# Kernel tuning notes

Measured on AMD Instinct MI355X. Metric: run time of the kernel, lower is better.

The kernel has to match this reference:

```python
import jax, jax.numpy as jnp
import numpy as np

B, C, D = 512, 100000, 512
MARGIN = 0.5  # ArcFace-style additive angular margin


def setup_inputs() -> dict:
    key = jax.random.key(0)
    k1, k2, k3 = jax.random.split(key, 3)
    embeddings = jax.random.normal(k1, (B, D), dtype=jnp.float32)
    labels = jax.random.randint(k2, (B,), 0, C, dtype=jnp.int32)
    weight = 0.01 * jax.random.normal(k3, (C, D), dtype=jnp.float32)  # torch.normal(0, 0.01, (C, D))
    return {"embeddings": embeddings, "labels": labels, "weight": weight}


def _l2_normalize(x, eps=1e-12):
    return x / jnp.maximum(jnp.linalg.norm(x, axis=-1, keepdims=True), eps)


def reference(embeddings, labels, weight):
    cos_m = jnp.cos(MARGIN)
    sin_m = jnp.sin(MARGIN)

    e = _l2_normalize(embeddings)          # (B, D)
    w = _l2_normalize(weight)              # (C, D)
    logits = jnp.clip(jnp.einsum('bd,cd->bc', e, w), -1.0, 1.0)  # (B, C) cosines

    bsz, ncls = logits.shape
    rows = jnp.arange(bsz)
    cos_t = logits[rows, labels]                                   # (B,) cos(theta_y)
    sin_t = jnp.sqrt(jnp.clip(1.0 - cos_t * cos_t, 0.0, None))     # sin(theta_y)
    cos_tm = cos_t * cos_m - sin_t * sin_m                         # cos(theta_y + m)
    sin_tm = sin_t * cos_m + cos_t * sin_m                         # sin(theta_y + m)

    # non-target class indices per row, ascending, skipping the target: (B, C-1)
    base = jnp.arange(ncls - 1)[None, :]
    nt_idx = base + (base >= labels[:, None]).astype(base.dtype)

    # margin_softmax: logits2 = cos(theta_j) - cos(theta_y + m) over non-target j
    nt_logits = jnp.take_along_axis(logits, nt_idx, axis=1)       # (B, C-1)
    logits2 = nt_logits - cos_tm[:, None]

    # no_grad block: weight_m is unit-norm point at angle theta_y+m from e,
    # so ||w_j - w_m||^2 = 2 - 2 <w_j, w_m>  (avoids materializing (B, C, D)).
    w_y = w[labels]                                                # (B, D)
    w_m = (-sin_m * e + sin_tm[:, None] * w_y) / sin_t[:, None]    # (B, D), unit norm
    sim = jnp.einsum('bd,cd->bc', w_m, w)                          # (B, C)
    nt_sim = jnp.take_along_axis(sim, nt_idx, axis=1)              # (B, C-1)
    diff_weight_norm = jax.lax.stop_gradient(
        jnp.sqrt(jnp.clip(2.0 - 2.0 * nt_sim, 0.0, None)))         # (B, C-1)

    e_logits = jnp.sum(jnp.exp(logits2 / diff_weight_norm), axis=1)  # (B,)
    return jnp.mean(jnp.log1p(e_logits))
```

## Files before the change

kernel.cpp:

```cpp
#include <hip/hip_runtime.h>
#include <hip/hip_fp8.h>
#include <math.h>

#define B_SZ 512
#define C_SZ 100000
#define D_SZ 512

#define BM 128
#define BN 128
#define BK 64
#define NTILES 782
#define MT 8
#define NBLK (NTILES * MT)
#define KSTEPS 8
#define DEPTH 3

typedef __attribute__((ext_vector_type(4))) float f32x4;
typedef __attribute__((ext_vector_type(16))) float f32x16;
typedef __attribute__((ext_vector_type(4))) int i32x4;
typedef __attribute__((ext_vector_type(8))) int i32x8;

#define UNITY_SCALE 0x7F7F7F7F

__device__ __forceinline__ void gload_lds16(const void* gptr, void* lptr) {
  __builtin_amdgcn_global_load_lds(
      (const __attribute__((address_space(1))) void*)gptr,
      (__attribute__((address_space(3))) void*)lptr,
      16, 0, 0);
}

__device__ __forceinline__ unsigned char f2fp8(float x) {
  __hip_fp8_e4m3 h(x);
  return (unsigned char)h.__x;
}
__device__ __forceinline__ float fp82f(unsigned int u) {
  __hip_fp8_e4m3 h;
  h.__x = (unsigned char)u;
  return (float)h;
}
__device__ __forceinline__ unsigned int pack4f8(float a, float b, float c, float d) {
  return (unsigned int)f2fp8(a) | ((unsigned int)f2fp8(b) << 8) |
         ((unsigned int)f2fp8(c) << 16) | ((unsigned int)f2fp8(d) << 24);
}

__global__ __launch_bounds__(256) void k_norm_w(const float* __restrict__ w,
                                                unsigned char* __restrict__ w8) {
  const int row = blockIdx.x * 4 + (threadIdx.x >> 6);
  const int lane = threadIdx.x & 63;
  const float4* wr = (const float4*)(w + (size_t)row * D_SZ);
  float4 v0 = wr[lane];
  float4 v1 = wr[64 + lane];
  float ss = v0.x*v0.x + v0.y*v0.y + v0.z*v0.z + v0.w*v0.w
           + v1.x*v1.x + v1.y*v1.y + v1.z*v1.z + v1.w*v1.w;
  #pragma unroll
  for (int o = 32; o; o >>= 1) ss += __shfl_xor(ss, o, 64);
  const float rn = __builtin_amdgcn_rsqf(fmaxf(ss, 1e-24f));
  unsigned int* out = (unsigned int*)(w8 + (size_t)row * D_SZ);
  out[lane] = pack4f8(v0.x * rn, v0.y * rn, v0.z * rn, v0.w * rn);
  out[64 + lane] = pack4f8(v1.x * rn, v1.y * rn, v1.z * rn, v1.w * rn);
}

__global__ __launch_bounds__(64) void k_prep(const float* __restrict__ e,
                                             const int* __restrict__ labels,
                                             const unsigned char* __restrict__ w8,
                                             unsigned char* __restrict__ A8,
                                             float4* __restrict__ params) {
  const int b = blockIdx.x;
  const int lane = threadIdx.x;
  const float4* er = (const float4*)(e + (size_t)b * D_SZ);
  float4 v0 = er[lane], v1 = er[64 + lane];
  float ss = v0.x*v0.x + v0.y*v0.y + v0.z*v0.z + v0.w*v0.w
           + v1.x*v1.x + v1.y*v1.y + v1.z*v1.z + v1.w*v1.w;
  #pragma unroll
  for (int o = 32; o; o >>= 1) ss += __shfl_xor(ss, o, 64);
  const float rn = __builtin_amdgcn_rsqf(fmaxf(ss, 1e-24f));
  v0.x *= rn; v0.y *= rn; v0.z *= rn; v0.w *= rn;
  v1.x *= rn; v1.y *= rn; v1.z *= rn; v1.w *= rn;

  unsigned int* arow_e = (unsigned int*)(A8 + (size_t)(2 * b) * D_SZ);
  arow_e[lane] = pack4f8(v0.x, v0.y, v0.z, v0.w);
  arow_e[64 + lane] = pack4f8(v1.x, v1.y, v1.z, v1.w);

  const int lab = labels[b];
  const unsigned int* wr = (const unsigned int*)(w8 + (size_t)lab * D_SZ);
  unsigned int w0 = wr[lane], w1 = wr[64 + lane];
  unsigned int* arow_w = (unsigned int*)(A8 + (size_t)(2 * b + 1) * D_SZ);
  arow_w[lane] = w0;
  arow_w[64 + lane] = w1;

  float d = v0.x * fp82f(w0 & 255) + v0.y * fp82f((w0 >> 8) & 255)
          + v0.z * fp82f((w0 >> 16) & 255) + v0.w * fp82f(w0 >> 24)
          + v1.x * fp82f(w1 & 255) + v1.y * fp82f((w1 >> 8) & 255)
          + v1.z * fp82f((w1 >> 16) & 255) + v1.w * fp82f(w1 >> 24);
  #pragma unroll
  for (int o = 32; o; o >>= 1) d += __shfl_xor(d, o, 64);

  if (lane == 0) {
    const float cos_m = 0.877582561890372716f;
    const float sin_m = 0.479425538604203000f;
    float cos_t = fminf(fmaxf(d, -1.0f), 1.0f);
    float sin_t = sqrtf(fmaxf(1.0f - cos_t * cos_t, 0.0f));
    float cos_tm = cos_t * cos_m - sin_t * sin_m;
    float sin_tm = sin_t * cos_m + cos_t * sin_m;
    float inv_st = 1.0f / fmaxf(sin_t, 1e-20f);
    params[b] = make_float4(cos_tm, sin_m * inv_st, sin_tm * inv_st, 0.0f);
  }
}

__device__ __forceinline__ float termf(float de, float dwy, float4 p, bool kill) {
  float c = fminf(fmaxf(de, -1.0f), 1.0f);
  float s = p.z * dwy - p.y * de;
  float x = fmaxf(fmaf(-2.0f, s, 2.0f), 1e-20f);
  float t = (c - p.x) * __builtin_amdgcn_rsqf(x);
  float r = __expf(t);
  return kill ? 0.0f : r;
}

__global__ __launch_bounds__(512, 4) void k_gemm(const unsigned char* __restrict__ A8,
                                                 const unsigned char* __restrict__ W8,
                                                 const float4* __restrict__ params,
                                                 const int* __restrict__ labels,
                                                 float* __restrict__ part) {
  __shared__ __align__(32) unsigned char At[DEPTH][BM * BK];
  __shared__ __align__(32) unsigned char Bt[DEPTH][BN * BK];
  __shared__ float ered[64];
  __shared__ float4 pl[64];
  __shared__ int ll[64];

  const int bid = blockIdx.x;
  const int p = (bid & 7) * (NBLK / 8) + (bid >> 3);
  const int nt = p >> 3, mt = p & 7;
  const int t = threadIdx.x;
  const int w = t >> 6, l = t & 63;
  const int m0 = mt * BM;
  const int n0 = nt * BN;
  const int b0 = mt * 64;

  if (t < 64) {
    ered[t] = 0.0f;
    pl[t] = params[b0 + t];
    ll[t] = labels[b0 + t];
  }

  const int kpart = ((t >> 5) & 1) * 32 + ((t >> 6) & 1) * 16;
  const int aoffs = (m0 + (t >> 7) * 32 + (t & 31)) * D_SZ + kpart;
  int brow_s = n0 + (t >> 7) * 32 + (t & 31);
  if (brow_s >= C_SZ) brow_s = C_SZ - 1;
  const int boffs = brow_s * D_SZ + kpart;

  f32x16 accA = {}, accB = {};
  const int fA = w & 3;
  const int fB0 = (w >> 2) * 2;
  const int hi = l >> 5;

#define STAGE(d, ts)                                                        \
  do {                                                                      \
    const int k0_ = (ts) * BK;                                              \
    gload_lds16(A8 + aoffs + k0_, (void*)(At[d] + t * 16));                 \
    gload_lds16(W8 + (size_t)(boffs + k0_), (void*)(Bt[d] + t * 16));       \
  } while (0)

  STAGE(0, 0);
  STAGE(1, 1);
  STAGE(2, 2);
  asm volatile("s_waitcnt vmcnt(4) lgkmcnt(0)" ::: "memory");
  __builtin_amdgcn_s_barrier();

  #pragma unroll
  for (int step = 0; step < KSTEPS; ++step) {
    const int d = step % DEPTH;
    i32x4 alo = *(const i32x4*)(At[d] + fA * 2048 + l * 16);
    i32x4 ahi = *(const i32x4*)(At[d] + fA * 2048 + 1024 + l * 16);
    i32x8 av = __builtin_shufflevector(alo, ahi, 0, 1, 2, 3, 4, 5, 6, 7);
    i32x4 b0lo = *(const i32x4*)(Bt[d] + fB0 * 2048 + l * 16);
    i32x4 b0hi = *(const i32x4*)(Bt[d] + fB0 * 2048 + 1024 + l * 16);
    i32x8 bv0 = __builtin_shufflevector(b0lo, b0hi, 0, 1, 2, 3, 4, 5, 6, 7);
    i32x4 b1lo = *(const i32x4*)(Bt[d] + (fB0 + 1) * 2048 + l * 16);
    i32x4 b1hi = *(const i32x4*)(Bt[d] + (fB0 + 1) * 2048 + 1024 + l * 16);
    i32x8 bv1 = __builtin_shufflevector(b1lo, b1hi, 0, 1, 2, 3, 4, 5, 6, 7);
    __builtin_amdgcn_s_setprio(1);
    accA = __builtin_amdgcn_mfma_scale_f32_32x32x64_f8f6f4(
        av, bv0, accA, 0, 0, 0, UNITY_SCALE, 0, UNITY_SCALE);
    accB = __builtin_amdgcn_mfma_scale_f32_32x32x64_f8f6f4(
        av, bv1, accB, 0, 0, 0, UNITY_SCALE, 0, UNITY_SCALE);
    __builtin_amdgcn_s_setprio(0);
    if (step < KSTEPS - 1) {
      asm volatile("s_waitcnt vmcnt(2)" ::: "memory");
      __builtin_amdgcn_s_barrier();
      if (step + DEPTH < KSTEPS)
        STAGE(d, step + DEPTH);
    }
  }
#undef STAGE

  #pragma unroll
  for (int rp = 0; rp < 8; ++rp) {
    const int r = 2 * rp;
    const int lb = fA * 16 + (rp & 1) + 4 * (rp >> 1) + 2 * hi;
    float4 pp = pl[lb];
    int lab = ll[lb];
    int j0 = n0 + fB0 * 32 + (l & 31);
    int j1 = j0 + 32;
    float s = termf(accA[r], accA[r + 1], pp, (j0 >= C_SZ) || (j0 == lab))
            + termf(accB[r], accB[r + 1], pp, (j1 >= C_SZ) || (j1 == lab));
    #pragma unroll
    for (int o = 1; o < 32; o <<= 1) s += __shfl_xor(s, o, 64);
    if ((l & 31) == 0) atomicAdd(&ered[lb], s);
  }
  __syncthreads();
  if (t < 64) part[(size_t)(b0 + t) * NTILES + nt] = ered[t];
}

__global__ __launch_bounds__(256) void k_rowsum(const float* __restrict__ part,
                                                float* __restrict__ rowsum) {
  const int b = blockIdx.x;
  float s = 0.0f;
  for (int i = threadIdx.x; i < NTILES; i += 256) s += part[(size_t)b * NTILES + i];
  #pragma unroll
  for (int o = 32; o; o >>= 1) s += __shfl_xor(s, o, 64);
  __shared__ float red[4];
  if ((threadIdx.x & 63) == 0) red[threadIdx.x >> 6] = s;
  __syncthreads();
  if (threadIdx.x == 0)
    rowsum[b] = log1pf(red[0] + red[1] + red[2] + red[3]);
}

__global__ __launch_bounds__(512) void k_final(const float* __restrict__ rowsum,
                                               float* __restrict__ out) {
  const int b = threadIdx.x;
  float v = rowsum[b];
  __shared__ float red[512];
  red[b] = v;
  __syncthreads();
  #pragma unroll
  for (int o = 256; o; o >>= 1) {
    if (b < o) red[b] += red[b + o];
    __syncthreads();
  }
  if (b == 0) out[0] = red[0] / (float)B_SZ;
}

extern "C" void kernel_launch(void* const* d_in, const int* in_sizes, int n_in,
                              void* d_out, int out_size, void* d_ws, size_t ws_size,
                              hipStream_t stream) {
  const float* emb = (const float*)d_in[0];
  const int* labels = (const int*)d_in[1];
  const float* w = (const float*)d_in[2];

  char* ws = (char*)d_ws;
  unsigned char* w8 = (unsigned char*)ws;
  size_t off = (size_t)C_SZ * D_SZ;
  unsigned char* A8 = (unsigned char*)(ws + off);
  off += (size_t)2 * B_SZ * D_SZ;
  float4* params = (float4*)(ws + off);
  off += (size_t)B_SZ * 16;
  float* part = (float*)(ws + off);
  off += (size_t)B_SZ * NTILES * 4;
  float* rowsum = (float*)(ws + off);
  off += (size_t)B_SZ * 4;

  k_norm_w<<<dim3(C_SZ / 4), dim3(256), 0, stream>>>(w, w8);
  k_prep<<<dim3(B_SZ), dim3(64), 0, stream>>>(emb, labels, w8, A8, params);
  k_gemm<<<dim3(NBLK), dim3(512), 0, stream>>>(A8, w8, params, labels, part);
  k_rowsum<<<dim3(B_SZ), dim3(256), 0, stream>>>(part, rowsum);
  k_final<<<dim3(1), dim3(512), 0, stream>>>(rowsum, (float*)d_out);
}
```

Before: 146.2 us.

## Halve block threads and give each wave a 2x2 MFMA sub-tile

Launches the fused GEMM+loss kernel with 256 threads instead of 512. Each wave now computes four 32x32 accumulators, reusing each loaded A and B fragment across two MFMAs, and each thread stages two A and two B chunks per k-step. This is meant to cut LDS reads per MFMA and per-block thread overhead. In exchange it raises register pressure and reduces waves available for latency hiding; the epilogue is duplicated per A sub-tile.

Result: slower. 158.8 us (+8.6%).

```diff
diff --git a/kernel.cpp b/kernel.cpp
--- a/kernel.cpp
+++ b/kernel.cpp
@@ -116,7 +116,7 @@
   return kill ? 0.0f : r;
 }
 
-__global__ __launch_bounds__(512, 4) void k_gemm(const unsigned char* __restrict__ A8,
+__global__ __launch_bounds__(256, 3) void k_gemm(const unsigned char* __restrict__ A8,
                                                  const unsigned char* __restrict__ W8,
                                                  const float4* __restrict__ params,
                                                  const int* __restrict__ labels,
@@ -143,49 +143,63 @@
   }
 
   const int kpart = ((t >> 5) & 1) * 32 + ((t >> 6) & 1) * 16;
-  const int aoffs = (m0 + (t >> 7) * 32 + (t & 31)) * D_SZ + kpart;
-  int brow_s = n0 + (t >> 7) * 32 + (t & 31);
-  if (brow_s >= C_SZ) brow_s = C_SZ - 1;
-  const int boffs = brow_s * D_SZ + kpart;
-
-  f32x16 accA = {}, accB = {};
-  const int fA = w & 3;
-  const int fB0 = (w >> 2) * 2;
+  const int aoffs0 = (m0 + (t >> 7) * 32 + (t & 31)) * D_SZ + kpart;
+  const int aoffs1 = aoffs0 + 64 * D_SZ;
+  int brow0 = n0 + (t >> 7) * 32 + (t & 31);
+  int brow1 = brow0 + 64;
+  if (brow0 >= C_SZ) brow0 = C_SZ - 1;
+  if (brow1 >= C_SZ) brow1 = C_SZ - 1;
+  const int boffs0 = brow0 * D_SZ + kpart;
+  const int boffs1 = brow1 * D_SZ + kpart;
+
+  f32x16 acc00 = {}, acc01 = {}, acc10 = {}, acc11 = {};
+  const int fA0 = (w & 1) * 2;
+  const int fB0 = (w >> 1) * 2;
   const int hi = l >> 5;
 
 #define STAGE(d, ts)                                                        \
   do {                                                                      \
     const int k0_ = (ts) * BK;                                              \
-    gload_lds16(A8 + aoffs + k0_, (void*)(At[d] + t * 16));                 \
-    gload_lds16(W8 + (size_t)(boffs + k0_), (void*)(Bt[d] + t * 16));       \
+    gload_lds16(A8 + aoffs0 + k0_, (void*)(At[d] + t * 16));                \
+    gload_lds16(A8 + aoffs1 + k0_, (void*)(At[d] + 4096 + t * 16));         \
+    gload_lds16(W8 + (size_t)(boffs0 + k0_), (void*)(Bt[d] + t * 16));      \
+    gload_lds16(W8 + (size_t)(boffs1 + k0_), (void*)(Bt[d] + 4096 + t * 16)); \
   } while (0)
 
   STAGE(0, 0);
   STAGE(1, 1);
   STAGE(2, 2);
-  asm volatile("s_waitcnt vmcnt(4) lgkmcnt(0)" ::: "memory");
+  asm volatile("s_waitcnt vmcnt(8) lgkmcnt(0)" ::: "memory");
   __builtin_amdgcn_s_barrier();
 
   #pragma unroll
   for (int step = 0; step < KSTEPS; ++step) {
     const int d = step % DEPTH;
-    i32x4 alo = *(const i32x4*)(At[d] + fA * 2048 + l * 16);
-    i32x4 ahi = *(const i32x4*)(At[d] + fA * 2048 + 1024 + l * 16);
-    i32x8 av = __builtin_shufflevector(alo, ahi, 0, 1, 2, 3, 4, 5, 6, 7);
-    i32x4 b0lo = *(const i32x4*)(Bt[d] + fB0 * 2048 + l * 16);
-    i32x4 b0hi = *(const i32x4*)(Bt[d] + fB0 * 2048 + 1024 + l * 16);
-    i32x8 bv0 = __builtin_shufflevector(b0lo, b0hi, 0, 1, 2, 3, 4, 5, 6, 7);
-    i32x4 b1lo = *(const i32x4*)(Bt[d] + (fB0 + 1) * 2048 + l * 16);
-    i32x4 b1hi = *(const i32x4*)(Bt[d] + (fB0 + 1) * 2048 + 1024 + l * 16);
-    i32x8 bv1 = __builtin_shufflevector(b1lo, b1hi, 0, 1, 2, 3, 4, 5, 6, 7);
+    i32x4 lo, hg;
+    lo = *(const i32x4*)(At[d] + fA0 * 2048 + l * 16);
+    hg = *(const i32x4*)(At[d] + fA0 * 2048 + 1024 + l * 16);
+    i32x8 av0 = __builtin_shufflevector(lo, hg, 0, 1, 2, 3, 4, 5, 6, 7);
+    lo = *(const i32x4*)(At[d] + (fA0 + 1) * 2048 + l * 16);
+    hg = *(const i32x4*)(At[d] + (fA0 + 1) * 2048 + 1024 + l * 16);
+    i32x8 av1 = __builtin_shufflevector(lo, hg, 0, 1, 2, 3, 4, 5, 6, 7);
+    lo = *(const i32x4*)(Bt[d] + fB0 * 2048 + l * 16);
+    hg = *(const i32x4*)(Bt[d] + fB0 * 2048 + 1024 + l * 16);
+    i32x8 bv0 = __builtin_shufflevector(lo, hg, 0, 1, 2, 3, 4, 5, 6, 7);
+    lo = *(const i32x4*)(Bt[d] + (fB0 + 1) * 2048 + l * 16);
+    hg = *(const i32x4*)(Bt[d] + (fB0 + 1) * 2048 + 1024 + l * 16);
+    i32x8 bv1 = __builtin_shufflevector(lo, hg, 0, 1, 2, 3, 4, 5, 6, 7);
     __builtin_amdgcn_s_setprio(1);
-    accA = __builtin_amdgcn_mfma_scale_f32_32x32x64_f8f6f4(
-        av, bv0, accA, 0, 0, 0, UNITY_SCALE, 0, UNITY_SCALE);
-    accB = __builtin_amdgcn_mfma_scale_f32_32x32x64_f8f6f4(
-        av, bv1, accB, 0, 0, 0, UNITY_SCALE, 0, UNITY_SCALE);
+    acc00 = __builtin_amdgcn_mfma_scale_f32_32x32x64_f8f6f4(
+        av0, bv0, acc00, 0, 0, 0, UNITY_SCALE, 0, UNITY_SCALE);
+    acc01 = __builtin_amdgcn_mfma_scale_f32_32x32x64_f8f6f4(
+        av0, bv1, acc01, 0, 0, 0, UNITY_SCALE, 0, UNITY_SCALE);
+    acc10 = __builtin_amdgcn_mfma_scale_f32_32x32x64_f8f6f4(
+        av1, bv0, acc10, 0, 0, 0, UNITY_SCALE, 0, UNITY_SCALE);
+    acc11 = __builtin_amdgcn_mfma_scale_f32_32x32x64_f8f6f4(
+        av1, bv1, acc11, 0, 0, 0, UNITY_SCALE, 0, UNITY_SCALE);
     __builtin_amdgcn_s_setprio(0);
     if (step < KSTEPS - 1) {
-      asm volatile("s_waitcnt vmcnt(2)" ::: "memory");
+      asm volatile("s_waitcnt vmcnt(4)" ::: "memory");
       __builtin_amdgcn_s_barrier();
       if (step + DEPTH < KSTEPS)
         STAGE(d, step + DEPTH);
@@ -196,16 +210,29 @@
   #pragma unroll
   for (int rp = 0; rp < 8; ++rp) {
     const int r = 2 * rp;
-    const int lb = fA * 16 + (rp & 1) + 4 * (rp >> 1) + 2 * hi;
-    float4 pp = pl[lb];
-    int lab = ll[lb];
-    int j0 = n0 + fB0 * 32 + (l & 31);
-    int j1 = j0 + 32;
-    float s = termf(accA[r], accA[r + 1], pp, (j0 >= C_SZ) || (j0 == lab))
-            + termf(accB[r], accB[r + 1], pp, (j1 >= C_SZ) || (j1 == lab));
-    #pragma unroll
-    for (int o = 1; o < 32; o <<= 1) s += __shfl_xor(s, o, 64);
-    if ((l & 31) == 0) atomicAdd(&ered[lb], s);
+    const int rowk = (rp & 1) + 4 * (rp >> 1) + 2 * hi;
+    const int j0 = n0 + fB0 * 32 + (l & 31);
+    const int j1 = j0 + 32;
+    {
+      const int lb = fA0 * 16 + rowk;
+      float4 pp = pl[lb];
+      int lab = ll[lb];
+      float s = termf(acc00[r], acc00[r + 1], pp, (j0 >= C_SZ) || (j0 == lab))
+              + termf(acc01[r], acc01[r + 1], pp, (j1 >= C_SZ) || (j1 == lab));
+      #pragma unroll
+      for (int o = 1; o < 32; o <<= 1) s += __shfl_xor(s, o, 64);
+      if ((l & 31) == 0) atomicAdd(&ered[lb], s);
+    }
+    {
+      const int lb = (fA0 + 1) * 16 + rowk;
+      float4 pp = pl[lb];
+      int lab = ll[lb];
+      float s = termf(acc10[r], acc10[r + 1], pp, (j0 >= C_SZ) || (j0 == lab))
+              + termf(acc11[r], acc11[r + 1], pp, (j1 >= C_SZ) || (j1 == lab));
+      #pragma unroll
+      for (int o = 1; o < 32; o <<= 1) s += __shfl_xor(s, o, 64);
+      if ((l & 31) == 0) atomicAdd(&ered[lb], s);
+    }
   }
   __syncthreads();
   if (t < 64) part[(size_t)(b0 + t) * NTILES + nt] = ered[t];
@@ -261,7 +288,7 @@
 
   k_norm_w<<<dim3(C_SZ / 4), dim3(256), 0, stream>>>(w, w8);
   k_prep<<<dim3(B_SZ), dim3(64), 0, stream>>>(emb, labels, w8, A8, params);
-  k_gemm<<<dim3(NBLK), dim3(512), 0, stream>>>(A8, w8, params, labels, part);
+  k_gemm<<<dim3(NBLK), dim3(256), 0, stream>>>(A8, w8, params, labels, part);
   k_rowsum<<<dim3(B_SZ), dim3(256), 0, stream>>>(part, rowsum);
   k_final<<<dim3(1), dim3(512), 0, stream>>>(rowsum, (float*)d_out);
 }
```

## Register double-buffer LDS fragments and restructure K-loop prefetch schedule

Applied to the files above, without the earlier changes.

Restructures the K loop so the fragments for the next step are read from LDS into registers while the MFMAs for the current step run. Global-to-LDS staging now issues two stages ahead inside the loop instead of a three-deep prologue, with a barrier every step. The goal is to hide LDS read latency behind matrix ops, at the cost of more registers for the second fragment set. It also enlarges the shared reduction arrays to 128 entries, which is unused by the visible code.

Result: slower. 167.3 us (+14.4%).

```diff
diff --git a/kernel.cpp b/kernel.cpp
--- a/kernel.cpp
+++ b/kernel.cpp
@@ -41,6 +41,12 @@
 __device__ __forceinline__ unsigned int pack4f8(float a, float b, float c, float d) {
   return (unsigned int)f2fp8(a) | ((unsigned int)f2fp8(b) << 8) |
          ((unsigned int)f2fp8(c) << 16) | ((unsigned int)f2fp8(d) << 24);
+}
+
+__device__ __forceinline__ i32x8 ld_frag(const unsigned char* base, int frag, int l) {
+  i32x4 lo = *(const i32x4*)(base + frag * 2048 + l * 16);
+  i32x4 hg = *(const i32x4*)(base + frag * 2048 + 1024 + l * 16);
+  return __builtin_shufflevector(lo, hg, 0, 1, 2, 3, 4, 5, 6, 7);
 }
 
 __global__ __launch_bounds__(256) void k_norm_w(const float* __restrict__ w,
@@ -123,9 +129,9 @@
                                                  float* __restrict__ part) {
   __shared__ __align__(32) unsigned char At[DEPTH][BM * BK];
   __shared__ __align__(32) unsigned char Bt[DEPTH][BN * BK];
-  __shared__ float ered[64];
-  __shared__ float4 pl[64];
-  __shared__ int ll[64];
+  __shared__ float ered[128];
+  __shared__ float4 pl[128];
+  __shared__ int ll[128];
 
   const int bid = blockIdx.x;
   const int p = (bid & 7) * (NBLK / 8) + (bid >> 3);
@@ -162,33 +168,42 @@
 
   STAGE(0, 0);
   STAGE(1, 1);
-  STAGE(2, 2);
-  asm volatile("s_waitcnt vmcnt(4) lgkmcnt(0)" ::: "memory");
+  asm volatile("s_waitcnt vmcnt(2)" ::: "memory");
   __builtin_amdgcn_s_barrier();
-
-  #pragma unroll
-  for (int step = 0; step < KSTEPS; ++step) {
-    const int d = step % DEPTH;
-    i32x4 alo = *(const i32x4*)(At[d] + fA * 2048 + l * 16);
-    i32x4 ahi = *(const i32x4*)(At[d] + fA * 2048 + 1024 + l * 16);
-    i32x8 av = __builtin_shufflevector(alo, ahi, 0, 1, 2, 3, 4, 5, 6, 7);
-    i32x4 b0lo = *(const i32x4*)(Bt[d] + fB0 * 2048 + l * 16);
-    i32x4 b0hi = *(const i32x4*)(Bt[d] + fB0 * 2048 + 1024 + l * 16);
-    i32x8 bv0 = __builtin_shufflevector(b0lo, b0hi, 0, 1, 2, 3, 4, 5, 6, 7);
-    i32x4 b1lo = *(const i32x4*)(Bt[d] + (fB0 + 1) * 2048 + l * 16);
-    i32x4 b1hi = *(const i32x4*)(Bt[d] + (fB0 + 1) * 2048 + 1024 + l * 16);
-    i32x8 bv1 = __builtin_shufflevector(b1lo, b1hi, 0, 1, 2, 3, 4, 5, 6, 7);
-    __builtin_amdgcn_s_setprio(1);
-    accA = __builtin_amdgcn_mfma_scale_f32_32x32x64_f8f6f4(
-        av, bv0, accA, 0, 0, 0, UNITY_SCALE, 0, UNITY_SCALE);
-    accB = __builtin_amdgcn_mfma_scale_f32_32x32x64_f8f6f4(
-        av, bv1, accB, 0, 0, 0, UNITY_SCALE, 0, UNITY_SCALE);
-    __builtin_amdgcn_s_setprio(0);
-    if (step < KSTEPS - 1) {
+  i32x8 av_c  = ld_frag(At[0], fA, l);
+  i32x8 bv0_c = ld_frag(Bt[0], fB0, l);
+  i32x8 bv1_c = ld_frag(Bt[0], fB0 + 1, l);
+
+  #pragma unroll
+  for (int s = 0; s < KSTEPS; ++s) {
+    if (s + 2 < KSTEPS) {
+      const int d2 = (s + 2) % DEPTH;
+      STAGE(d2, s + 2);
+    }
+    if (s < KSTEPS - 2)
       asm volatile("s_waitcnt vmcnt(2)" ::: "memory");
-      __builtin_amdgcn_s_barrier();
-      if (step + DEPTH < KSTEPS)
-        STAGE(d, step + DEPTH);
+    else
+      asm volatile("s_waitcnt vmcnt(0)" ::: "memory");
+    __builtin_amdgcn_s_barrier();
+    if (s < KSTEPS - 1) {
+      const int dn = (s + 1) % DEPTH;
+      i32x8 av_n  = ld_frag(At[dn], fA, l);
+      i32x8 bv0_n = ld_frag(Bt[dn], fB0, l);
+      i32x8 bv1_n = ld_frag(Bt[dn], fB0 + 1, l);
+      __builtin_amdgcn_s_setprio(1);
+      accA = __builtin_amdgcn_mfma_scale_f32_32x32x64_f8f6f4(
+          av_c, bv0_c, accA, 0, 0, 0, UNITY_SCALE, 0, UNITY_SCALE);
+      accB = __builtin_amdgcn_mfma_scale_f32_32x32x64_f8f6f4(
+          av_c, bv1_c, accB, 0, 0, 0, UNITY_SCALE, 0, UNITY_SCALE);
+      __builtin_amdgcn_s_setprio(0);
+      av_c = av_n; bv0_c = bv0_n; bv1_c = bv1_n;
+    } else {
+      __builtin_amdgcn_s_setprio(1);
+      accA = __builtin_amdgcn_mfma_scale_f32_32x32x64_f8f6f4(
+          av_c, bv0_c, accA, 0, 0, 0, UNITY_SCALE, 0, UNITY_SCALE);
+      accB = __builtin_amdgcn_mfma_scale_f32_32x32x64_f8f6f4(
+          av_c, bv1_c, accB, 0, 0, 0, UNITY_SCALE, 0, UNITY_SCALE);
+      __builtin_amdgcn_s_setprio(0);
     }
   }
 #undef STAGE
```
